# Performance work log

Measured on AMD Instinct MI355X. Metric: run time of the kernel, lower is better.

Reference implementation:

```python
import jax, jax.numpy as jnp
import numpy as np

N_PARENT = 16384
N_CHILD = 8 * N_PARENT  # nearest upsample, nempty=False: 8 children per parent
C = 128
K = 27  # 3x3x3 octree conv stencil


def setup_inputs() -> dict:
    key = jax.random.key(0)
    k1, k2, k3, k4 = jax.random.split(key, 4)
    x = jax.random.normal(k1, (N_PARENT, C), dtype=jnp.float32)
    # conv weight per stencil offset, fan-in scaled init
    w = jax.random.normal(k2, (K, C, C), dtype=jnp.float32) / np.sqrt(K * C)
    b = jnp.zeros((C,), dtype=jnp.float32)
    # neighbor table at depth+1; -1 marks missing neighbors (zero-padded)
    neigh = jax.random.randint(k3, (N_CHILD, K), -1, N_CHILD, dtype=jnp.int32)
    return {"x": x, "w": w, "b": b, "neigh": neigh}


def reference(x, w, b, neigh):
    # OctreeUpsample(nearest, nempty=False): copy each parent feature to its
    # 8 contiguous children at depth+1.
    xu = jnp.repeat(x, 8, axis=0)  # [N_child, C]
    # OctreeConv: gather 27 neighbors (missing -> 0), then GEMM + bias.
    valid = neigh >= 0  # [N_child, 27]
    g = jnp.where(valid[..., None], xu[jnp.clip(neigh, 0)], 0.0)  # [N_child, 27, C]
    out = jnp.einsum('nkc,kcd->nd', g, w) + b  # [N_child, C]
    return out
```

## Files before the change

### kernel.cpp

```cpp
#include <hip/hip_runtime.h>
#include <hip/hip_bf16.h>

#define N_PARENT 16384
#define N_CHILD (8 * N_PARENT)
#define CC 128
#define KK 27

#define BM 128
#define BK 64
#define NSTAGE (KK * 2)

#define XB_OFF 0
#define XB_ELEMS (N_PARENT * CC)
#define WT_OFF XB_ELEMS
#define WT_ELEMS (KK * CC * CC)
#define ZR_OFF (WT_OFF + WT_ELEMS)
#define ZR_ELEMS 128

typedef __attribute__((ext_vector_type(8))) __bf16 bf16x8;
typedef __attribute__((ext_vector_type(4))) float f32x4;

__device__ __forceinline__ void gll16(const void* g, void* l) {
  __builtin_amdgcn_global_load_lds(
      (const __attribute__((address_space(1))) unsigned int*)g,
      (__attribute__((address_space(3))) unsigned int*)l,
      16, 0, 0);
}

__global__ void prep_kernel(const float* __restrict__ x,
                            const float* __restrict__ w,
                            __hip_bfloat16* __restrict__ ws) {
  const int stride = gridDim.x * blockDim.x;
  const int tid = blockIdx.x * blockDim.x + threadIdx.x;
  for (int i = tid; i < XB_ELEMS; i += stride)
    ws[XB_OFF + i] = __float2bfloat16(x[i]);
  for (int j = tid; j < WT_ELEMS; j += stride) {
    const int k = j / (CC * CC);
    const int rem = j - k * CC * CC;
    const int d = rem >> 7;
    const int c = rem & 127;
    ws[WT_OFF + j] = __float2bfloat16(w[k * CC * CC + c * CC + d]);
  }
  if (tid < ZR_ELEMS) ws[ZR_OFF + tid] = __float2bfloat16(0.0f);
}

__global__ __launch_bounds__(256, 2) void upconv_kernel(
    const int* __restrict__ neigh,
    const __hip_bfloat16* __restrict__ ws,
    const float* __restrict__ bias,
    float* __restrict__ out) {
  __shared__ __align__(16) __hip_bfloat16 As[2][BM * BK];
  __shared__ __align__(16) __hip_bfloat16 Bs[2][CC * BK];
  __shared__ short ridx[BM * KK];

  const __hip_bfloat16* xb = ws + XB_OFF;
  const __hip_bfloat16* wT = ws + WT_OFF;
  const __hip_bfloat16* zr = ws + ZR_OFF;

  const int tid = threadIdx.x;
  const int wv = tid >> 6;
  const int l = tid & 63;
  const int wr = wv >> 1;
  const int wc = wv & 1;
  const int row0 = blockIdx.x * BM;

  for (int j = tid; j < BM * KK; j += 256) {
    const int nv = neigh[row0 * KK + j];
    ridx[j] = (short)((nv >= 0) ? (nv >> 3) : -1);
  }
  __syncthreads();

  const int lr = l & 15;
  const int lk = (l >> 4) * 8;
  const int lrow = l >> 3;
  const int scol = ((l & 7) ^ lrow) * 8;

  f32x4 acc[4][4] = {};

  auto stage = [&](int buf, int s) {
    const int k = s >> 1;
    const int hOff = (s & 1) << 6;
#pragma unroll
    for (int i = 0; i < 4; ++i) {
      const int rg = wv * 32 + i * 8;
      const int rr = rg + lrow;
      const int ix = (int)ridx[rr * KK + k];
      const __hip_bfloat16* ga =
          (ix >= 0) ? (xb + (size_t)ix * CC + hOff + scol) : (zr + scol);
      gll16(ga, &As[buf][rg * BK]);
      const __hip_bfloat16* gb =
          wT + (size_t)k * (CC * CC) + (size_t)rr * CC + hOff + scol;
      gll16(gb, &Bs[buf][rg * BK]);
    }
  };

  auto compute = [&](int buf) {
    const int sw = (lr & 7) * 8;
#pragma unroll
    for (int kc = 0; kc < 2; ++kc) {
      const int ce = (kc * 32 + lk) ^ sw;
      bf16x8 a[4], bb[4];
#pragma unroll
      for (int m = 0; m < 4; ++m)
        a[m] = *reinterpret_cast<const bf16x8*>(
            &As[buf][(wr * 64 + m * 16 + lr) * BK + ce]);
#pragma unroll
      for (int n = 0; n < 4; ++n)
        bb[n] = *reinterpret_cast<const bf16x8*>(
            &Bs[buf][(wc * 64 + n * 16 + lr) * BK + ce]);
#pragma unroll
      for (int m = 0; m < 4; ++m)
#pragma unroll
        for (int n = 0; n < 4; ++n)
          acc[m][n] =
              __builtin_amdgcn_mfma_f32_16x16x32_bf16(a[m], bb[n], acc[m][n],
                                                      0, 0, 0);
    }
  };

  stage(0, 0);
  for (int s = 0; s < NSTAGE; ++s) {
    const int cur = s & 1;
    if (s + 1 < NSTAGE) {
      stage(cur ^ 1, s + 1);
      asm volatile("s_waitcnt vmcnt(8)" ::: "memory");
    } else {
      asm volatile("s_waitcnt vmcnt(0)" ::: "memory");
    }
    __builtin_amdgcn_s_barrier();
    __builtin_amdgcn_s_setprio(1);
    compute(cur);
    __builtin_amdgcn_s_setprio(0);
    __builtin_amdgcn_s_barrier();
  }

  float bv[4];
#pragma unroll
  for (int n = 0; n < 4; ++n) bv[n] = bias[wc * 64 + n * 16 + lr];
  const int rbase = row0 + wr * 64 + (l >> 4) * 4;
#pragma unroll
  for (int m = 0; m < 4; ++m)
#pragma unroll
    for (int n = 0; n < 4; ++n)
#pragma unroll
      for (int q = 0; q < 4; ++q)
        out[(size_t)(rbase + m * 16 + q) * CC + wc * 64 + n * 16 + lr] =
            acc[m][n][q] + bv[n];
}

extern "C" void kernel_launch(void* const* d_in, const int* in_sizes, int n_in,
                              void* d_out, int out_size, void* d_ws,
                              size_t ws_size, hipStream_t stream) {
  const float* x = (const float*)d_in[0];
  const float* w = (const float*)d_in[1];
  const float* b = (const float*)d_in[2];
  const int* neigh = (const int*)d_in[3];
  __hip_bfloat16* ws = (__hip_bfloat16*)d_ws;
  float* out = (float*)d_out;

  hipLaunchKernelGGL(prep_kernel, dim3(512), dim3(256), 0, stream, x, w, ws);
  hipLaunchKernelGGL(upconv_kernel, dim3(N_CHILD / BM), dim3(256), 0, stream,
                     neigh, ws, b, out);
}
```

Baseline: 146.6 us.

## Use 256-row tiles, 8 waves, triple-buffered LDS with interleaved loads and MFMA

Doubles the tile to 256 output rows and runs 512 threads (8 waves) per block, so each staged weight tile is reused across twice as many gathered rows. LDS buffering goes from double to triple, with loads prefetched two stages ahead. Each stage's compute is split into four MFMA phases, and the gather and weight loads for the next-but-one stage are issued between them to overlap memory with matrix math. Shared memory grows to about 160KB, so only one block fits per CU, and the extra barriers add synchronization cost.

```diff
diff --git a/kernel.cpp b/kernel.cpp
--- a/kernel.cpp
+++ b/kernel.cpp
@@ -6,9 +6,11 @@
 #define CC 128
 #define KK 27
 
-#define BM 128
+#define BM 256
+#define BN 128
 #define BK 64
 #define NSTAGE (KK * 2)
+#define NBUF 3
 
 #define XB_OFF 0
 #define XB_ELEMS (N_PARENT * CC)
@@ -44,13 +46,13 @@
   if (tid < ZR_ELEMS) ws[ZR_OFF + tid] = __float2bfloat16(0.0f);
 }
 
-__global__ __launch_bounds__(256, 2) void upconv_kernel(
+__global__ __launch_bounds__(512, 2) void upconv_kernel(
     const int* __restrict__ neigh,
     const __hip_bfloat16* __restrict__ ws,
     const float* __restrict__ bias,
     float* __restrict__ out) {
-  __shared__ __align__(16) __hip_bfloat16 As[2][BM * BK];
-  __shared__ __align__(16) __hip_bfloat16 Bs[2][CC * BK];
+  __shared__ __align__(16) __hip_bfloat16 As[NBUF][BM * BK];
+  __shared__ __align__(16) __hip_bfloat16 Bs[NBUF][BN * BK];
   __shared__ short ridx[BM * KK];
 
   const __hip_bfloat16* xb = ws + XB_OFF;
@@ -64,7 +66,7 @@
   const int wc = wv & 1;
   const int row0 = blockIdx.x * BM;
 
-  for (int j = tid; j < BM * KK; j += 256) {
+  for (int j = tid; j < BM * KK; j += 512) {
     const int nv = neigh[row0 * KK + j];
     ridx[j] = (short)((nv >= 0) ? (nv >> 3) : -1);
   }
@@ -74,63 +76,113 @@
   const int lk = (l >> 4) * 8;
   const int lrow = l >> 3;
   const int scol = ((l & 7) ^ lrow) * 8;
+  const int sw = (lr & 7) * 8;
 
   f32x4 acc[4][4] = {};
-
-  auto stage = [&](int buf, int s) {
-    const int k = s >> 1;
-    const int hOff = (s & 1) << 6;
-#pragma unroll
-    for (int i = 0; i < 4; ++i) {
-      const int rg = wv * 32 + i * 8;
-      const int rr = rg + lrow;
-      const int ix = (int)ridx[rr * KK + k];
-      const __hip_bfloat16* ga =
-          (ix >= 0) ? (xb + (size_t)ix * CC + hOff + scol) : (zr + scol);
-      gll16(ga, &As[buf][rg * BK]);
-      const __hip_bfloat16* gb =
-          wT + (size_t)k * (CC * CC) + (size_t)rr * CC + hOff + scol;
-      gll16(gb, &Bs[buf][rg * BK]);
+  bf16x8 a[4], b[2];
+
+  auto stageA = [&](int bf, int h, int r, int rid) {
+    const __hip_bfloat16* ga =
+        (rid >= 0) ? (xb + (size_t)rid * CC + h + scol) : (zr + scol);
+    gll16(ga, &As[bf][(r * 64 + wv * 8) * BK]);
+  };
+  auto stageB = [&](int bf, int k, int h, int r) {
+    const int d = r * 64 + wv * 8 + lrow;
+    gll16(wT + (size_t)k * (CC * CC) + (size_t)d * CC + h + scol,
+          &Bs[bf][(r * 64 + wv * 8) * BK]);
+  };
+
+  auto readA = [&](int bf, int kc) {
+#pragma unroll
+    for (int m = 0; m < 4; ++m)
+      a[m] = *reinterpret_cast<const bf16x8*>(
+          &As[bf][(wr * 64 + m * 16 + lr) * BK + ((kc * 32 + lk) ^ sw)]);
+  };
+  auto readB = [&](int bf, int kc, int nh) {
+#pragma unroll
+    for (int i = 0; i < 2; ++i)
+      b[i] = *reinterpret_cast<const bf16x8*>(
+          &Bs[bf][(wc * 64 + (nh * 2 + i) * 16 + lr) * BK +
+                  ((kc * 32 + lk) ^ sw)]);
+  };
+  auto mmac = [&](int nh) {
+#pragma unroll
+    for (int m = 0; m < 4; ++m)
+#pragma unroll
+      for (int i = 0; i < 2; ++i)
+        acc[m][nh * 2 + i] = __builtin_amdgcn_mfma_f32_16x16x32_bf16(
+            a[m], b[i], acc[m][nh * 2 + i], 0, 0, 0);
+  };
+
+  {
+    int rid0[4];
+#pragma unroll
+    for (int r = 0; r < 4; ++r)
+      rid0[r] = ridx[(r * 64 + wv * 8 + lrow) * KK + 0];
+    stageB(0, 0, 0, 0);  stageB(0, 0, 0, 1);
+    stageA(0, 0, 0, rid0[0]);  stageA(0, 0, 1, rid0[1]);
+    stageA(0, 0, 2, rid0[2]);  stageA(0, 0, 3, rid0[3]);
+    stageB(1, 0, 64, 0); stageB(1, 0, 64, 1);
+    stageA(1, 64, 0, rid0[0]); stageA(1, 64, 1, rid0[1]);
+    stageA(1, 64, 2, rid0[2]); stageA(1, 64, 3, rid0[3]);
+  }
+  asm volatile("s_waitcnt vmcnt(6)" ::: "memory");
+  __syncthreads();
+
+  for (int s = 0; s < NSTAGE; ++s) {
+    const int bf = s % 3;
+    const int sb = (s + 2) % 3;
+    const int k2 = (s + 2) >> 1;
+    const int h2 = (s & 1) << 6;
+    const bool st = (s + 2) < NSTAGE;
+
+    int ridv[4] = {-1, -1, -1, -1};
+
+    readA(bf, 0);
+    readB(bf, 0, 0);
+    if (st) {
+#pragma unroll
+      for (int r = 0; r < 4; ++r)
+        ridv[r] = ridx[(r * 64 + wv * 8 + lrow) * KK + k2];
+      stageB(sb, k2, h2, 0);
+      stageB(sb, k2, h2, 1);
     }
-  };
-
-  auto compute = [&](int buf) {
-    const int sw = (lr & 7) * 8;
-#pragma unroll
-    for (int kc = 0; kc < 2; ++kc) {
-      const int ce = (kc * 32 + lk) ^ sw;
-      bf16x8 a[4], bb[4];
-#pragma unroll
-      for (int m = 0; m < 4; ++m)
-        a[m] = *reinterpret_cast<const bf16x8*>(
-            &As[buf][(wr * 64 + m * 16 + lr) * BK + ce]);
-#pragma unroll
-      for (int n = 0; n < 4; ++n)
-        bb[n] = *reinterpret_cast<const bf16x8*>(
-            &Bs[buf][(wc * 64 + n * 16 + lr) * BK + ce]);
-#pragma unroll
-      for (int m = 0; m < 4; ++m)
-#pragma unroll
-        for (int n = 0; n < 4; ++n)
-          acc[m][n] =
-              __builtin_amdgcn_mfma_f32_16x16x32_bf16(a[m], bb[n], acc[m][n],
-                                                      0, 0, 0);
-    }
-  };
-
-  stage(0, 0);
-  for (int s = 0; s < NSTAGE; ++s) {
-    const int cur = s & 1;
-    if (s + 1 < NSTAGE) {
-      stage(cur ^ 1, s + 1);
-      asm volatile("s_waitcnt vmcnt(8)" ::: "memory");
-    } else {
+    __builtin_amdgcn_s_barrier();
+    asm volatile("s_waitcnt lgkmcnt(0)" ::: "memory");
+    __builtin_amdgcn_s_setprio(1);
+    mmac(0);
+    __builtin_amdgcn_s_setprio(0);
+    __builtin_amdgcn_s_barrier();
+
+    readB(bf, 0, 1);
+    if (st) { stageA(sb, h2, 0, ridv[0]); stageA(sb, h2, 1, ridv[1]); }
+    __builtin_amdgcn_s_barrier();
+    asm volatile("s_waitcnt lgkmcnt(0)" ::: "memory");
+    __builtin_amdgcn_s_setprio(1);
+    mmac(1);
+    __builtin_amdgcn_s_setprio(0);
+    __builtin_amdgcn_s_barrier();
+
+    readA(bf, 1);
+    readB(bf, 1, 0);
+    if (st) { stageA(sb, h2, 2, ridv[2]); stageA(sb, h2, 3, ridv[3]); }
+    __builtin_amdgcn_s_barrier();
+    asm volatile("s_waitcnt lgkmcnt(0)" ::: "memory");
+    __builtin_amdgcn_s_setprio(1);
+    mmac(0);
+    __builtin_amdgcn_s_setprio(0);
+    __builtin_amdgcn_s_barrier();
+
+    readB(bf, 1, 1);
+    __builtin_amdgcn_s_barrier();
+    asm volatile("s_waitcnt lgkmcnt(0)" ::: "memory");
+    __builtin_amdgcn_s_setprio(1);
+    mmac(1);
+    __builtin_amdgcn_s_setprio(0);
+    if (s < NSTAGE - 2)
+      asm volatile("s_waitcnt vmcnt(6)" ::: "memory");
+    else
       asm volatile("s_waitcnt vmcnt(0)" ::: "memory");
-    }
-    __builtin_amdgcn_s_barrier();
-    __builtin_amdgcn_s_setprio(1);
-    compute(cur);
-    __builtin_amdgcn_s_setprio(0);
     __builtin_amdgcn_s_barrier();
   }
 
@@ -159,6 +211,6 @@
   float* out = (float*)d_out;
 
   hipLaunchKernelGGL(prep_kernel, dim3(512), dim3(256), 0, stream, x, w, ws);
-  hipLaunchKernelGGL(upconv_kernel, dim3(N_CHILD / BM), dim3(256), 0, stream,
+  hipLaunchKernelGGL(upconv_kernel, dim3(N_CHILD / BM), dim3(512), 0, stream,
                      neigh, ws, b, out);
 }
```

New measurement: 147.8 us. About the same (+0.8%).

## Load gathered A operand directly into registers, keep only weights in LDS

Applied to the files above, without the earlier changes.

The gathered activation tile no longer goes through shared memory. Each wave now loads its own A fragments from global memory straight into registers, double-buffered as aP and aN across the two K-halves of each stencil offset, while the weight tile is still staged in LDS with global_load_lds. This removes the LDS writes and reads for A and half of the LDS footprint. In exchange, waves that share rows load the same A data twice, the 16-byte gather loads are less coalesced, and 64 extra VGPRs are held, which may strain the two-blocks-per-CU occupancy target.

```diff
diff --git a/kernel.cpp b/kernel.cpp
--- a/kernel.cpp
+++ b/kernel.cpp
@@ -7,6 +7,7 @@
 #define KK 27
 
 #define BM 128
+#define BN 128
 #define BK 64
 #define NSTAGE (KK * 2)
 
@@ -49,8 +50,7 @@
     const __hip_bfloat16* __restrict__ ws,
     const float* __restrict__ bias,
     float* __restrict__ out) {
-  __shared__ __align__(16) __hip_bfloat16 As[2][BM * BK];
-  __shared__ __align__(16) __hip_bfloat16 Bs[2][CC * BK];
+  __shared__ __align__(16) __hip_bfloat16 Bs[2][BN * BK];
   __shared__ short ridx[BM * KK];
 
   const __hip_bfloat16* xb = ws + XB_OFF;
@@ -71,66 +71,82 @@
   __syncthreads();
 
   const int lr = l & 15;
-  const int lk = (l >> 4) * 8;
+  const int lk8 = (l >> 4) * 8;
   const int lrow = l >> 3;
   const int scol = ((l & 7) ^ lrow) * 8;
+  const int sw = (lr & 7) * 8;
 
   f32x4 acc[4][4] = {};
+  bf16x8 aP[8], aN[8];
 
-  auto stage = [&](int buf, int s) {
-    const int k = s >> 1;
-    const int hOff = (s & 1) << 6;
+  auto stageB = [&](int buf, int k, int h) {
 #pragma unroll
     for (int i = 0; i < 4; ++i) {
-      const int rg = wv * 32 + i * 8;
-      const int rr = rg + lrow;
-      const int ix = (int)ridx[rr * KK + k];
-      const __hip_bfloat16* ga =
-          (ix >= 0) ? (xb + (size_t)ix * CC + hOff + scol) : (zr + scol);
-      gll16(ga, &As[buf][rg * BK]);
-      const __hip_bfloat16* gb =
-          wT + (size_t)k * (CC * CC) + (size_t)rr * CC + hOff + scol;
-      gll16(gb, &Bs[buf][rg * BK]);
+      const int dg = wv * 32 + i * 8;
+      gll16(wT + (size_t)k * (CC * CC) + (size_t)(dg + lrow) * CC + h + scol,
+            &Bs[buf][dg * BK]);
     }
   };
 
-  auto compute = [&](int buf) {
-    const int sw = (lr & 7) * 8;
+  int rid[4];
+  auto loadRid = [&](int k) {
+#pragma unroll
+    for (int m = 0; m < 4; ++m)
+      rid[m] = (int)ridx[(wr * 64 + m * 16 + lr) * KK + k];
+  };
+
+  auto loadA = [&](bf16x8* A, int h) {
+#pragma unroll
+    for (int m = 0; m < 4; ++m) {
+      const __hip_bfloat16* base =
+          (rid[m] >= 0) ? (xb + (size_t)rid[m] * CC + h + lk8) : (zr + lk8);
+      A[m * 2 + 0] = *reinterpret_cast<const bf16x8*>(base);
+      A[m * 2 + 1] = *reinterpret_cast<const bf16x8*>(base + 32);
+    }
+  };
+
+  auto compute = [&](int buf, const bf16x8* A) {
 #pragma unroll
     for (int kc = 0; kc < 2; ++kc) {
-      const int ce = (kc * 32 + lk) ^ sw;
-      bf16x8 a[4], bb[4];
-#pragma unroll
-      for (int m = 0; m < 4; ++m)
-        a[m] = *reinterpret_cast<const bf16x8*>(
-            &As[buf][(wr * 64 + m * 16 + lr) * BK + ce]);
+      bf16x8 b[4];
+      const int ce = (kc * 32 + lk8) ^ sw;
 #pragma unroll
       for (int n = 0; n < 4; ++n)
-        bb[n] = *reinterpret_cast<const bf16x8*>(
+        b[n] = *reinterpret_cast<const bf16x8*>(
             &Bs[buf][(wc * 64 + n * 16 + lr) * BK + ce]);
+      __builtin_amdgcn_s_setprio(1);
 #pragma unroll
       for (int m = 0; m < 4; ++m)
 #pragma unroll
         for (int n = 0; n < 4; ++n)
-          acc[m][n] =
-              __builtin_amdgcn_mfma_f32_16x16x32_bf16(a[m], bb[n], acc[m][n],
-                                                      0, 0, 0);
+          acc[m][n] = __builtin_amdgcn_mfma_f32_16x16x32_bf16(
+              A[m * 2 + kc], b[n], acc[m][n], 0, 0, 0);
+      __builtin_amdgcn_s_setprio(0);
     }
   };
 
-  stage(0, 0);
-  for (int s = 0; s < NSTAGE; ++s) {
-    const int cur = s & 1;
-    if (s + 1 < NSTAGE) {
-      stage(cur ^ 1, s + 1);
-      asm volatile("s_waitcnt vmcnt(8)" ::: "memory");
+  loadRid(0);
+  stageB(0, 0, 0);
+  loadA(aP, 0);
+
+  for (int k = 0; k < KK; ++k) {
+    stageB(1, k, 64);
+    loadA(aN, 64);
+    asm volatile("s_waitcnt vmcnt(12)" ::: "memory");
+    __builtin_amdgcn_s_barrier();
+    compute(0, aP);
+    __builtin_amdgcn_s_barrier();
+
+    if (k + 1 < KK) {
+      loadRid(k + 1);
+      stageB(0, k + 1, 0);
+      loadA(aP, 0);
+      asm volatile("s_waitcnt vmcnt(12)" ::: "memory");
     } else {
       asm volatile("s_waitcnt vmcnt(0)" ::: "memory");
     }
     __builtin_amdgcn_s_barrier();
-    __builtin_amdgcn_s_setprio(1);
-    compute(cur);
-    __builtin_amdgcn_s_setprio(0);
+    compute(1, aN);
     __builtin_amdgcn_s_barrier();
   }
 
```

Result: slower. 243.7 us (+66.2%).
